# Performance work log

Measured on AMD Instinct MI355X. Metric: run time of the kernel, lower is better.

Reference implementation:

```python
import jax, jax.numpy as jnp
import numpy as np
from jax import lax

B, T, I, H, O = 256, 512, 64, 128, 2  # batch, seq_len, input_size, hidden_size, output_size


def gru_layer(x, Wih, Whh, bih, bhh, reverse):
    # x: [B,T,in_dim], Wih: [3H,in_dim], Whh: [3H,H]; PyTorch gate order: r, z, n
    xw = jnp.einsum('bti,gi->btg', x, Wih) + bih  # precompute input projections [B,T,3H]

    def step(h, xw_t):
        gh = h @ Whh.T + bhh  # [B,3H]
        r = jax.nn.sigmoid(xw_t[:, :H] + gh[:, :H])
        z = jax.nn.sigmoid(xw_t[:, H:2 * H] + gh[:, H:2 * H])
        n = jnp.tanh(xw_t[:, 2 * H:] + r * gh[:, 2 * H:])
        h_new = (1.0 - z) * n + z * h
        return h_new, h_new

    h0 = jnp.zeros((x.shape[0], H), x.dtype)
    _, hs = lax.scan(step, h0, jnp.swapaxes(xw, 0, 1), reverse=reverse)
    # lax.scan with reverse=True stacks outputs aligned to original time order,
    # matching PyTorch's bidirectional GRU output layout.
    return jnp.swapaxes(hs, 0, 1)  # [B,T,H]


def gru_forward(x, params, fc_w, fc_b):
    h = x
    for (Wf, Uf, bf, cf, Wb, Ub, bb, cb) in params:
        fwd = gru_layer(h, Wf, Uf, bf, cf, reverse=False)
        bwd = gru_layer(h, Wb, Ub, bb, cb, reverse=True)
        h = jnp.concatenate([fwd, bwd], axis=-1)  # [B,T,2H]
    last = jax.nn.relu(h[:, -1, :])  # relu then take last timestep (equivalent order)
    return last @ fc_w.T + fc_b  # [B,O]


def setup_inputs() -> dict:
    key = jax.random.key(0)
    ks = iter(jax.random.split(key, 24))
    s = 1.0 / np.sqrt(H)  # PyTorch GRU init scale
    u = lambda shape: jax.random.uniform(next(ks), shape, jnp.float32, -s, s)
    inp = {"x": jax.random.normal(next(ks), (B, T, I), jnp.float32)}
    for l, in_dim in enumerate([I, 2 * H]):
        for d in ("f", "b"):
            inp[f"Wih{l}{d}"] = u((3 * H, in_dim))
            inp[f"Whh{l}{d}"] = u((3 * H, H))
            inp[f"bih{l}{d}"] = u((3 * H,))
            inp[f"bhh{l}{d}"] = u((3 * H,))
    inp["fc_w"] = u((O, 2 * H))
    inp["fc_b"] = u((O,))
    return inp


def reference(x, Wih0f, Whh0f, bih0f, bhh0f, Wih0b, Whh0b, bih0b, bhh0b,
              Wih1f, Whh1f, bih1f, bhh1f, Wih1b, Whh1b, bih1b, bhh1b,
              fc_w, fc_b):
    params = [(Wih0f, Whh0f, bih0f, bhh0f, Wih0b, Whh0b, bih0b, bhh0b),
              (Wih1f, Whh1f, bih1f, bhh1f, Wih1b, Whh1b, bih1b, bhh1b)]
    return gru_forward(x, params, fc_w, fc_b)
```

## Files before the change

### kernel.cpp

```cpp
#include <hip/hip_runtime.h>
#include <hip/hip_fp16.h>

#define B_  256
#define T_  512
#define I_  64
#define H_  128
#define G_  384
#define HC  256

#define O_OUT0 0ull
#define O_XW1  67108864ull
#define O_X16  O_XW1
#define O_WP   167772160ull
#define O_H1F  (O_WP + 196608ull)
#define O_WF16 (O_H1F + 131072ull)

typedef _Float16 h8 __attribute__((ext_vector_type(8)));
typedef _Float16 h2 __attribute__((ext_vector_type(2)));
typedef float    f4 __attribute__((ext_vector_type(4)));

#define MFMA16 __builtin_amdgcn_mfma_f32_16x16x32_f16

__device__ __forceinline__ float sigm(float x)   { return __builtin_amdgcn_rcpf(1.f + __expf(-x)); }
__device__ __forceinline__ float tanh_f(float x) { return 1.f - 2.f * __builtin_amdgcn_rcpf(1.f + __expf(2.f * x)); }

__device__ __forceinline__ void bar_lds() {
    asm volatile("s_waitcnt lgkmcnt(0)\n\ts_barrier" ::: "memory");
}

__device__ __forceinline__ h8 load_w8(const float* src) {
    f4 a = *(const f4*)src;
    f4 b = *(const f4*)(src + 4);
    h8 v;
    v[0]=(_Float16)a[0]; v[1]=(_Float16)a[1]; v[2]=(_Float16)a[2]; v[3]=(_Float16)a[3];
    v[4]=(_Float16)b[0]; v[5]=(_Float16)b[1]; v[6]=(_Float16)b[2]; v[7]=(_Float16)b[3];
    return v;
}

__global__ void prep(const float* __restrict__ x, _Float16* __restrict__ x16,
                     const float* __restrict__ Wf, _Float16* __restrict__ wf16,
                     const float* __restrict__ W1b, __half2* __restrict__ wp) {
    const int bid = blockIdx.x;
    const int tid = threadIdx.x;
    if (bid < 4096) {
        int i = bid * 256 + tid;
        const float* s = x + (size_t)i * 8;
        f4 a = *(const f4*)s, b = *(const f4*)(s + 4);
        h8 v;
        v[0]=(_Float16)a[0]; v[1]=(_Float16)a[1]; v[2]=(_Float16)a[2]; v[3]=(_Float16)a[3];
        v[4]=(_Float16)b[0]; v[5]=(_Float16)b[1]; v[6]=(_Float16)b[2]; v[7]=(_Float16)b[3];
        *(h8*)(x16 + (size_t)i * 8) = v;
    } else if (bid < 4144) {
        int i = (bid - 4096) * 256 + tid;
        const float* s = Wf + (size_t)i * 8;
        f4 a = *(const f4*)s, b = *(const f4*)(s + 4);
        h8 v;
        v[0]=(_Float16)a[0]; v[1]=(_Float16)a[1]; v[2]=(_Float16)a[2]; v[3]=(_Float16)a[3];
        v[4]=(_Float16)b[0]; v[5]=(_Float16)b[1]; v[6]=(_Float16)b[2]; v[7]=(_Float16)b[3];
        *(h8*)(wf16 + (size_t)i * 8) = v;
    } else {
        int i = (bid - 4144) * 256 + tid;
        int c = i % G_;
        int k2 = i / G_;
        wp[i] = __halves2half2(__float2half(W1b[c * 256 + 2 * k2]),
                               __float2half(W1b[c * 256 + 2 * k2 + 1]));
    }
}

__launch_bounds__(512, 1)
__global__ void scan_l0(const _Float16* __restrict__ x16,
                        const float* __restrict__ Wih_f, const float* __restrict__ Whh_f,
                        const float* __restrict__ bih_f, const float* __restrict__ bhh_f,
                        const float* __restrict__ Wih_b, const float* __restrict__ Whh_b,
                        const float* __restrict__ bih_b, const float* __restrict__ bhh_b,
                        _Float16* __restrict__ out0) {
    __shared__ __align__(16) _Float16 s_h[2][16 * 128];

    const int tid  = threadIdx.x;
    const int lane = tid & 63;
    const int w    = tid >> 6;
    const int dir  = blockIdx.y;
    const int b0   = blockIdx.x * 4;

    const float* Wih = dir ? Wih_b : Wih_f;
    const float* Whh = dir ? Whh_b : Whh_f;
    const float* bih = dir ? bih_b : bih_f;
    const float* bhh = dir ? bhh_b : bhh_f;

    for (int i = tid; i < 2 * 16 * 128; i += 512) ((_Float16*)s_h)[i] = (_Float16)0.f;

    const int ln15 = lane & 15;
    const int lq   = lane >> 4;
    const int col  = 16 * w + ln15;

    h8 bh[3][4], bx[3][2];
    float seedR = bih[col] + bhh[col];
    float seedZ = bih[H_ + col] + bhh[H_ + col];
    float bihN  = bih[2 * H_ + col];
    float bhhN  = bhh[2 * H_ + col];
#pragma unroll
    for (int g = 0; g < 3; g++) {
        int n = g * H_ + col;
#pragma unroll
        for (int kt = 0; kt < 4; kt++) bh[g][kt] = load_w8(Whh + (size_t)n * H_ + kt * 32 + lq * 8);
#pragma unroll
        for (int kt = 0; kt < 2; kt++) bx[g][kt] = load_w8(Wih + (size_t)n * I_ + kt * 32 + lq * 8);
    }
    const int arow = ln15 & 12;
    int offh[4];
#pragma unroll
    for (int kt = 0; kt < 4; kt++)
        offh[kt] = arow * 128 + (((kt * 4 + lq) ^ arow) & 15) * 8;
    const int row0  = lq * 4;
    const int offw0 = row0 * 128 + ((((col >> 3) ^ row0) & 15)) * 8 + (col & 7);

    const _Float16* xbase = x16 + ((size_t)(b0 + (ln15 >> 2)) * T_) * I_ + lq * 8;

    const f4 z4 = (f4){0.f, 0.f, 0.f, 0.f};
    const f4 sR4 = (f4){seedR, seedR, seedR, seedR};
    const f4 sZ4 = (f4){seedZ, seedZ, seedZ, seedZ};
    const f4 sXn4 = (f4){bihN, bihN, bihN, bihN};
    const f4 sHn4 = (f4){bhhN, bhhN, bhhN, bhhN};

    _Float16* op = out0 + ((size_t)(b0 + lq) * T_ + (dir ? (T_ - 1) : 0)) * HC + dir * H_ + col;
    const int ostep = dir ? -HC : HC;
    const _Float16* xpA = xbase + (size_t)(dir ? (T_ - 4) : 3) * I_;
    const _Float16* xpB = xbase + (size_t)(dir ? (T_ - 5) : 4) * I_;
    const int xstep = dir ? -(2 * I_) : (2 * I_);

    float hF = 0.f;
    float xr0, xz0, xn0, xr1, xz1, xn1;
    h8 xvA0, xvA1, xvB0, xvB1;
    {
        int t0 = dir ? (T_ - 1) : 0;
        int t1 = dir ? (T_ - 2) : 1;
        int t2 = dir ? (T_ - 3) : 2;
        h8 xc0 = *(const h8*)(xbase + (size_t)t0 * I_);
        h8 xc1 = *(const h8*)(xbase + (size_t)t0 * I_ + 32);
        xvA0 = *(const h8*)(xbase + (size_t)t1 * I_);
        xvA1 = *(const h8*)(xbase + (size_t)t1 * I_ + 32);
        xvB0 = *(const h8*)(xbase + (size_t)t2 * I_);
        xvB1 = *(const h8*)(xbase + (size_t)t2 * I_ + 32);
        f4 aXr = sR4, aXz = sZ4, aXn = sXn4;
        aXr = MFMA16(xc0, bx[0][0], aXr, 0, 0, 0);
        aXz = MFMA16(xc0, bx[1][0], aXz, 0, 0, 0);
        aXn = MFMA16(xc0, bx[2][0], aXn, 0, 0, 0);
        aXr = MFMA16(xc1, bx[0][1], aXr, 0, 0, 0);
        aXz = MFMA16(xc1, bx[1][1], aXz, 0, 0, 0);
        aXn = MFMA16(xc1, bx[2][1], aXn, 0, 0, 0);
        xr0 = aXr[0]; xz0 = aXz[0]; xn0 = aXn[0];
    }
    __syncthreads();

#pragma unroll 1
    for (int t = 0; t < T_; t += 2) {
        {
            h8 ah0 = *(const h8*)&s_h[0][offh[0]];
            h8 ah1 = *(const h8*)&s_h[0][offh[1]];
            h8 ah2 = *(const h8*)&s_h[0][offh[2]];
            h8 ah3 = *(const h8*)&s_h[0][offh[3]];
            f4 hRa = z4, hRb = z4, hZa = z4, hZb = z4, hNa = sHn4, hNb = z4;
            hRa = MFMA16(ah0, bh[0][0], hRa, 0, 0, 0);
            hZa = MFMA16(ah0, bh[1][0], hZa, 0, 0, 0);
            hNa = MFMA16(ah0, bh[2][0], hNa, 0, 0, 0);
            hRb = MFMA16(ah2, bh[0][2], hRb, 0, 0, 0);
            hZb = MFMA16(ah2, bh[1][2], hZb, 0, 0, 0);
            hNb = MFMA16(ah2, bh[2][2], hNb, 0, 0, 0);
            hRa = MFMA16(ah1, bh[0][1], hRa, 0, 0, 0);
            hZa = MFMA16(ah1, bh[1][1], hZa, 0, 0, 0);
            hNa = MFMA16(ah1, bh[2][1], hNa, 0, 0, 0);
            hRb = MFMA16(ah3, bh[0][3], hRb, 0, 0, 0);
            hZb = MFMA16(ah3, bh[1][3], hZb, 0, 0, 0);
            hNb = MFMA16(ah3, bh[2][3], hNb, 0, 0, 0);
            float r = sigm(xr0 + hRa[0] + hRb[0]);
            float z = sigm(xz0 + hZa[0] + hZb[0]);
            float n = tanh_f(xn0 + r * (hNa[0] + hNb[0]));
            float h = n + z * (hF - n);
            hF = h;
            s_h[1][offw0] = (_Float16)h;
            *op = (_Float16)h; op += ostep;
            {
                f4 aXr = sR4, aXz = sZ4, aXn = sXn4;
                aXr = MFMA16(xvA0, bx[0][0], aXr, 0, 0, 0);
                aXz = MFMA16(xvA0, bx[1][0], aXz, 0, 0, 0);
                aXn = MFMA16(xvA0, bx[2][0], aXn, 0, 0, 0);
                aXr = MFMA16(xvA1, bx[0][1], aXr, 0, 0, 0);
                aXz = MFMA16(xvA1, bx[1][1], aXz, 0, 0, 0);
                aXn = MFMA16(xvA1, bx[2][1], aXn, 0, 0, 0);
                xr1 = aXr[0]; xz1 = aXz[0]; xn1 = aXn[0];
            }
            if (t + 3 < T_) {
                xvA0 = *(const h8*)(xpA);
                xvA1 = *(const h8*)(xpA + 32);
                xpA += xstep;
            }
            bar_lds();
        }
        {
            h8 ah0 = *(const h8*)&s_h[1][offh[0]];
            h8 ah1 = *(const h8*)&s_h[1][offh[1]];
            h8 ah2 = *(const h8*)&s_h[1][offh[2]];
            h8 ah3 = *(const h8*)&s_h[1][offh[3]];
            f4 hRa = z4, hRb = z4, hZa = z4, hZb = z4, hNa = sHn4, hNb = z4;
            hRa = MFMA16(ah0, bh[0][0], hRa, 0, 0, 0);
            hZa = MFMA16(ah0, bh[1][0], hZa, 0, 0, 0);
            hNa = MFMA16(ah0, bh[2][0], hNa, 0, 0, 0);
            hRb = MFMA16(ah2, bh[0][2], hRb, 0, 0, 0);
            hZb = MFMA16(ah2, bh[1][2], hZb, 0, 0, 0);
            hNb = MFMA16(ah2, bh[2][2], hNb, 0, 0, 0);
            hRa = MFMA16(ah1, bh[0][1], hRa, 0, 0, 0);
            hZa = MFMA16(ah1, bh[1][1], hZa, 0, 0, 0);
            hNa = MFMA16(ah1, bh[2][1], hNa, 0, 0, 0);
            hRb = MFMA16(ah3, bh[0][3], hRb, 0, 0, 0);
            hZb = MFMA16(ah3, bh[1][3], hZb, 0, 0, 0);
            hNb = MFMA16(ah3, bh[2][3], hNb, 0, 0, 0);
            float r = sigm(xr1 + hRa[0] + hRb[0]);
            float z = sigm(xz1 + hZa[0] + hZb[0]);
            float n = tanh_f(xn1 + r * (hNa[0] + hNb[0]));
            float h = n + z * (hF - n);
            hF = h;
            s_h[0][offw0] = (_Float16)h;
            *op = (_Float16)h; op += ostep;
            if (t + 2 < T_) {
                f4 aXr = sR4, aXz = sZ4, aXn = sXn4;
                aXr = MFMA16(xvB0, bx[0][0], aXr, 0, 0, 0);
                aXz = MFMA16(xvB0, bx[1][0], aXz, 0, 0, 0);
                aXn = MFMA16(xvB0, bx[2][0], aXn, 0, 0, 0);
                aXr = MFMA16(xvB1, bx[0][1], aXr, 0, 0, 0);
                aXz = MFMA16(xvB1, bx[1][1], aXz, 0, 0, 0);
                aXn = MFMA16(xvB1, bx[2][1], aXn, 0, 0, 0);
                xr0 = aXr[0]; xz0 = aXz[0]; xn0 = aXn[0];
            }
            if (t + 4 < T_) {
                xvB0 = *(const h8*)(xpB);
                xvB1 = *(const h8*)(xpB + 32);
                xpB += xstep;
            }
            bar_lds();
        }
    }
}

__launch_bounds__(256, 1)
__global__ void gemm_xw1(const _Float16* __restrict__ A,
                         const _Float16* __restrict__ Bw,
                         const float* __restrict__ bias,
                         _Float16* __restrict__ C) {
    __shared__ __align__(16) _Float16 sA[2][64 * 64];
    __shared__ __align__(16) _Float16 sB[2][384 * 64];
    const int tid  = threadIdx.x;
    const int lane = tid & 63;
    const int w    = tid >> 6;
    const int wm   = w & 1, wn = w >> 1;
    const int ln15 = lane & 15, lq = lane >> 4;
    const size_t m0 = (size_t)blockIdx.x * 64;

    f4 acc[2][12] = {};

    int aRow[2], aG[2], aOff[2];
#pragma unroll
    for (int k = 0; k < 2; k++) {
        int idx = k * 256 + tid;
        aRow[k] = idx >> 3; aG[k] = idx & 7;
        aOff[k] = aRow[k] * 64 + ((aG[k] ^ (aRow[k] & 7)) & 7) * 8;
    }
    int bRow[12], bG[12], bOff[12];
#pragma unroll
    for (int k = 0; k < 12; k++) {
        int idx = k * 256 + tid;
        bRow[k] = idx >> 3; bG[k] = idx & 7;
        bOff[k] = bRow[k] * 64 + ((bG[k] ^ (bRow[k] & 7)) & 7) * 8;
    }
    int offA[2][2], offB[12][2];
#pragma unroll
    for (int mt = 0; mt < 2; mt++)
#pragma unroll
        for (int kt = 0; kt < 2; kt++) {
            int row = wm * 32 + mt * 16 + ln15;
            offA[mt][kt] = row * 64 + (((kt * 4 + lq) ^ (row & 7)) & 7) * 8;
        }
#pragma unroll
    for (int nt = 0; nt < 12; nt++)
#pragma unroll
        for (int kt = 0; kt < 2; kt++) {
            int row = wn * 192 + nt * 16 + ln15;
            offB[nt][kt] = row * 64 + (((kt * 4 + lq) ^ (row & 7)) & 7) * 8;
        }

    {
        h8 av[2], bv[12];
#pragma unroll
        for (int k = 0; k < 2; k++) av[k] = *(const h8*)(A + (m0 + aRow[k]) * 256 + aG[k] * 8);
#pragma unroll
        for (int k = 0; k < 12; k++) bv[k] = *(const h8*)(Bw + (size_t)bRow[k] * 256 + bG[k] * 8);
#pragma unroll
        for (int k = 0; k < 2; k++) *(h8*)&sA[0][aOff[k]] = av[k];
#pragma unroll
        for (int k = 0; k < 12; k++) *(h8*)&sB[0][bOff[k]] = bv[k];
        bar_lds();
    }

#pragma unroll
    for (int c = 0; c < 4; c++) {
        const int cur = c & 1;
        h8 av[2], bv[12];
        if (c < 3) {
#pragma unroll
            for (int k = 0; k < 2; k++)
                av[k] = *(const h8*)(A + (m0 + aRow[k]) * 256 + (c + 1) * 64 + aG[k] * 8);
#pragma unroll
            for (int k = 0; k < 12; k++)
                bv[k] = *(const h8*)(Bw + (size_t)bRow[k] * 256 + (c + 1) * 64 + bG[k] * 8);
        }
#pragma unroll
        for (int kt = 0; kt < 2; kt++) {
            h8 af0 = *(const h8*)&sA[cur][offA[0][kt]];
            h8 af1 = *(const h8*)&sA[cur][offA[1][kt]];
#pragma unroll
            for (int nt = 0; nt < 12; nt++) {
                h8 bf = *(const h8*)&sB[cur][offB[nt][kt]];
                acc[0][nt] = MFMA16(af0, bf, acc[0][nt], 0, 0, 0);
                acc[1][nt] = MFMA16(af1, bf, acc[1][nt], 0, 0, 0);
            }
        }
        if (c < 3) {
#pragma unroll
            for (int k = 0; k < 2; k++) *(h8*)&sA[cur ^ 1][aOff[k]] = av[k];
#pragma unroll
            for (int k = 0; k < 12; k++) *(h8*)&sB[cur ^ 1][bOff[k]] = bv[k];
            bar_lds();
        }
    }
#pragma unroll
    for (int nt = 0; nt < 12; nt++) {
        int col = wn * 192 + nt * 16 + ln15;
        float bb = bias[col];
        int pcol = (col < 256) ? ((col & 127) * 2 + (col >> 7)) : col;
#pragma unroll
        for (int mt = 0; mt < 2; mt++) {
            size_t row = m0 + wm * 32 + mt * 16 + lq * 4;
#pragma unroll
            for (int reg = 0; reg < 4; reg++)
                C[(row + reg) * G_ + pcol] = (_Float16)(acc[mt][nt][reg] + bb);
        }
    }
}

__launch_bounds__(512, 1)
__global__ void scan_l1(const _Float16* __restrict__ xw1,
                        const float* __restrict__ Whh,
                        const float* __restrict__ bhh,
                        float* __restrict__ h1f) {
    __shared__ __align__(16) _Float16 s_h[2][16 * 128];

    const int tid  = threadIdx.x;
    const int lane = tid & 63;
    const int w    = tid >> 6;
    const int b0   = blockIdx.x * 4;

    for (int i = tid; i < 2 * 16 * 128; i += 512) ((_Float16*)s_h)[i] = (_Float16)0.f;

    const int ln15 = lane & 15;
    const int lq   = lane >> 4;
    const int col  = 16 * w + ln15;

    h8 bh[3][4];
    float bhhF[3];
#pragma unroll
    for (int g = 0; g < 3; g++) {
        int n = g * H_ + col;
        bhhF[g] = bhh[n];
#pragma unroll
        for (int kt = 0; kt < 4; kt++) bh[g][kt] = load_w8(Whh + (size_t)n * H_ + kt * 32 + lq * 8);
    }
    const int arow = ln15 & 12;
    int offh[4];
#pragma unroll
    for (int kt = 0; kt < 4; kt++)
        offh[kt] = arow * 128 + (((kt * 4 + lq) ^ arow) & 15) * 8;
    const int row0  = lq * 4;
    const int offw0 = row0 * 128 + ((((col >> 3) ^ row0) & 15)) * 8 + (col & 7);

    const _Float16* rzbase = xw1 + ((size_t)(b0 + lq) * T_) * G_ + 2 * col;
    const _Float16* nbase  = xw1 + ((size_t)(b0 + lq) * T_) * G_ + 256 + col;

    const f4 z4 = (f4){0.f, 0.f, 0.f, 0.f};
    const f4 sR4 = (f4){bhhF[0], bhhF[0], bhhF[0], bhhF[0]};
    const f4 sZ4 = (f4){bhhF[1], bhhF[1], bhhF[1], bhhF[1]};
    const f4 sN4 = (f4){bhhF[2], bhhF[2], bhhF[2], bhhF[2]};

    __syncthreads();

    float hF = 0.f;
    h2 rzA = *(const h2*)(rzbase);
    h2 rzB = *(const h2*)(rzbase + G_);
    _Float16 nA = *nbase;
    _Float16 nB = *(nbase + G_);
    const _Float16* rzP2 = rzbase + 2 * G_;
    const _Float16* nP2  = nbase  + 2 * G_;
    const _Float16* rzP3 = rzbase + 3 * G_;
    const _Float16* nP3  = nbase  + 3 * G_;

#pragma unroll 1
    for (int s = 0; s < T_; s += 2) {
        {
            h8 ah0 = *(const h8*)&s_h[0][offh[0]];
            h8 ah1 = *(const h8*)&s_h[0][offh[1]];
            h8 ah2 = *(const h8*)&s_h[0][offh[2]];
            h8 ah3 = *(const h8*)&s_h[0][offh[3]];
            float xr = (float)rzA[0], xz = (float)rzA[1], xn = (float)nA;
            if (s + 2 < T_) {
                rzA = *(const h2*)rzP2;
                nA  = *nP2;
                rzP2 += 2 * G_; nP2 += 2 * G_;
            }
            f4 hRa = sR4, hRb = z4, hZa = sZ4, hZb = z4, hNa = sN4, hNb = z4;
            hRa = MFMA16(ah0, bh[0][0], hRa, 0, 0, 0);
            hZa = MFMA16(ah0, bh[1][0], hZa, 0, 0, 0);
            hNa = MFMA16(ah0, bh[2][0], hNa, 0, 0, 0);
            hRb = MFMA16(ah2, bh[0][2], hRb, 0, 0, 0);
            hZb = MFMA16(ah2, bh[1][2], hZb, 0, 0, 0);
            hNb = MFMA16(ah2, bh[2][2], hNb, 0, 0, 0);
            hRa = MFMA16(ah1, bh[0][1], hRa, 0, 0, 0);
            hZa = MFMA16(ah1, bh[1][1], hZa, 0, 0, 0);
            hNa = MFMA16(ah1, bh[2][1], hNa, 0, 0, 0);
            hRb = MFMA16(ah3, bh[0][3], hRb, 0, 0, 0);
            hZb = MFMA16(ah3, bh[1][3], hZb, 0, 0, 0);
            hNb = MFMA16(ah3, bh[2][3], hNb, 0, 0, 0);
            float r = sigm(xr + hRa[0] + hRb[0]);
            float z = sigm(xz + hZa[0] + hZb[0]);
            float n = tanh_f(xn + r * (hNa[0] + hNb[0]));
            float h = n + z * (hF - n);
            hF = h;
            s_h[1][offw0] = (_Float16)h;
            bar_lds();
        }
        {
            h8 ah0 = *(const h8*)&s_h[1][offh[0]];
            h8 ah1 = *(const h8*)&s_h[1][offh[1]];
            h8 ah2 = *(const h8*)&s_h[1][offh[2]];
            h8 ah3 = *(const h8*)&s_h[1][offh[3]];
            float xr = (float)rzB[0], xz = (float)rzB[1], xn = (float)nB;
            if (s + 3 < T_) {
                rzB = *(const h2*)rzP3;
                nB  = *nP3;
                rzP3 += 2 * G_; nP3 += 2 * G_;
            }
            f4 hRa = sR4, hRb = z4, hZa = sZ4, hZb = z4, hNa = sN4, hNb = z4;
            hRa = MFMA16(ah0, bh[0][0], hRa, 0, 0, 0);
            hZa = MFMA16(ah0, bh[1][0], hZa, 0, 0, 0);
            hNa = MFMA16(ah0, bh[2][0], hNa, 0, 0, 0);
            hRb = MFMA16(ah2, bh[0][2], hRb, 0, 0, 0);
            hZb = MFMA16(ah2, bh[1][2], hZb, 0, 0, 0);
            hNb = MFMA16(ah2, bh[2][2], hNb, 0, 0, 0);
            hRa = MFMA16(ah1, bh[0][1], hRa, 0, 0, 0);
            hZa = MFMA16(ah1, bh[1][1], hZa, 0, 0, 0);
            hNa = MFMA16(ah1, bh[2][1], hNa, 0, 0, 0);
            hRb = MFMA16(ah3, bh[0][3], hRb, 0, 0, 0);
            hZb = MFMA16(ah3, bh[1][3], hZb, 0, 0, 0);
            hNb = MFMA16(ah3, bh[2][3], hNb, 0, 0, 0);
            float r = sigm(xr + hRa[0] + hRb[0]);
            float z = sigm(xz + hZa[0] + hZb[0]);
            float n = tanh_f(xn + r * (hNa[0] + hNb[0]));
            float h = n + z * (hF - n);
            hF = h;
            s_h[0][offw0] = (_Float16)h;
            bar_lds();
        }
    }
    h1f[(size_t)(b0 + lq) * H_ + col] = hF;
}

__launch_bounds__(384)
__global__ void final_k(const _Float16* __restrict__ out0,
                        const float* __restrict__ h1f,
                        const __half2* __restrict__ w1b,
                        const float* __restrict__ bih1b, const float* __restrict__ bhh1b,
                        const float* __restrict__ fcw, const float* __restrict__ fcb,
                        float* __restrict__ out) {
    __shared__ __align__(16) float s_x1[HC];
    __shared__ __align__(16) float s_xw[G_];
    __shared__ __align__(16) float s_hc[HC];
    __shared__ float s_red[8];
    const int tid = threadIdx.x;
    const int b = blockIdx.x;
    if (tid < HC)
        s_x1[tid] = (float)out0[((size_t)b * T_ + (T_ - 1)) * HC + tid];
    __syncthreads();
    {
        float acc0 = 0.f, acc1 = 0.f;
        const float2* xv = (const float2*)s_x1;
#pragma unroll 8
        for (int k2 = 0; k2 < 128; k2 += 2) {
            float2 w0 = __half22float2(w1b[k2 * G_ + tid]);
            float2 w1 = __half22float2(w1b[(k2 + 1) * G_ + tid]);
            float2 a0 = xv[k2], a1 = xv[k2 + 1];
            acc0 += a0.x * w0.x + a0.y * w0.y;
            acc1 += a1.x * w1.x + a1.y * w1.y;
        }
        s_xw[tid] = bih1b[tid] + acc0 + acc1;
    }
    __syncthreads();
    if (tid < H_) {
        int j = tid;
        float rg = sigm(s_xw[j] + bhh1b[j]);
        float zg = sigm(s_xw[H_ + j] + bhh1b[H_ + j]);
        float ng = tanh_f(s_xw[2 * H_ + j] + rg * bhh1b[2 * H_ + j]);
        float hb = (1.f - zg) * ng;
        s_hc[H_ + j] = fmaxf(hb, 0.f);
        s_hc[j] = fmaxf(h1f[(size_t)b * H_ + j], 0.f);
    }
    __syncthreads();
    if (tid < HC) {
        float hv = s_hc[tid];
        float p0 = hv * fcw[tid];
        float p1 = hv * fcw[HC + tid];
#pragma unroll
        for (int off = 32; off; off >>= 1) {
            p0 += __shfl_down(p0, off);
            p1 += __shfl_down(p1, off);
        }
        if ((tid & 63) == 0) { s_red[(tid >> 6) * 2] = p0; s_red[(tid >> 6) * 2 + 1] = p1; }
    }
    __syncthreads();
    if (tid == 0) {
        out[b * 2 + 0] = fcb[0] + s_red[0] + s_red[2] + s_red[4] + s_red[6];
        out[b * 2 + 1] = fcb[1] + s_red[1] + s_red[3] + s_red[5] + s_red[7];
    }
}

extern "C" void kernel_launch(void* const* d_in, const int* in_sizes, int n_in,
                              void* d_out, int out_size, void* d_ws, size_t ws_size,
                              hipStream_t stream) {
    (void)in_sizes; (void)n_in; (void)out_size; (void)ws_size;
    const float* x     = (const float*)d_in[0];
    const float* Wih0f = (const float*)d_in[1];
    const float* Whh0f = (const float*)d_in[2];
    const float* bih0f = (const float*)d_in[3];
    const float* bhh0f = (const float*)d_in[4];
    const float* Wih0b = (const float*)d_in[5];
    const float* Whh0b = (const float*)d_in[6];
    const float* bih0b = (const float*)d_in[7];
    const float* bhh0b = (const float*)d_in[8];
    const float* Wih1f = (const float*)d_in[9];
    const float* Whh1f = (const float*)d_in[10];
    const float* bih1f = (const float*)d_in[11];
    const float* bhh1f = (const float*)d_in[12];
    const float* Wih1b = (const float*)d_in[13];
    const float* bih1b = (const float*)d_in[15];
    const float* bhh1b = (const float*)d_in[16];
    const float* fcw   = (const float*)d_in[17];
    const float* fcb   = (const float*)d_in[18];

    char* ws = (char*)d_ws;
    _Float16* out0 = (_Float16*)(ws + O_OUT0);
    _Float16* xw1  = (_Float16*)(ws + O_XW1);
    _Float16* x16  = (_Float16*)(ws + O_X16);
    __half2*  wp   = (__half2*)(ws + O_WP);
    float*    h1f  = (float*)(ws + O_H1F);
    _Float16* wf16 = (_Float16*)(ws + O_WF16);
    float*    out  = (float*)d_out;

    prep<<<4336, 256, 0, stream>>>(x, x16, Wih1f, wf16, Wih1b, wp);

    scan_l0<<<dim3(64, 2), 512, 0, stream>>>(x16, Wih0f, Whh0f, bih0f, bhh0f,
                                             Wih0b, Whh0b, bih0b, bhh0b, out0);

    gemm_xw1<<<2048, 256, 0, stream>>>(out0, wf16, bih1f, xw1);

    scan_l1<<<64, 512, 0, stream>>>(xw1, Whh1f, bhh1f, h1f);

    final_k<<<256, 384, 0, stream>>>(out0, h1f, wp, bih1b, bhh1b, fcw, fcb, out);
}
```

Measured before the change: 576.0 us.

## Batch two timesteps per x-projection MFMA and halve scan_l1 waves

In scan_l0, the input-projection MFMA now packs rows from two consecutive timesteps into one 16x16 tile. Lanes pick their timestep by a bit of the lane index, and accumulator elements 0 and 2 are used, so one set of six MFMAs covers two steps instead of one. In scan_l1, each wave now computes two 16-column hidden tiles, so the block drops from 8 waves to 4. This cuts the wave count that takes part in every per-step barrier, at the cost of more per-wave MFMA work and register pressure on the serial recurrence path.

```diff
diff --git a/kernel.cpp b/kernel.cpp
--- a/kernel.cpp
+++ b/kernel.cpp
@@ -114,33 +114,28 @@
     const int row0  = lq * 4;
     const int offw0 = row0 * 128 + ((((col >> 3) ^ row0) & 15)) * 8 + (col & 7);
 
-    const _Float16* xbase = x16 + ((size_t)(b0 + (ln15 >> 2)) * T_) * I_ + lq * 8;
-
     const f4 z4 = (f4){0.f, 0.f, 0.f, 0.f};
     const f4 sR4 = (f4){seedR, seedR, seedR, seedR};
     const f4 sZ4 = (f4){seedZ, seedZ, seedZ, seedZ};
     const f4 sXn4 = (f4){bihN, bihN, bihN, bihN};
     const f4 sHn4 = (f4){bhhN, bhhN, bhhN, bhhN};
 
+    const int tbit = (ln15 >> 1) & 1;
+    const _Float16* xpb = x16 + ((size_t)(b0 + (ln15 >> 2)) * T_ + (dir ? (T_ - 1 - tbit) : tbit)) * I_ + lq * 8;
+    const int xIterStep = dir ? -(2 * I_) : (2 * I_);
+
     _Float16* op = out0 + ((size_t)(b0 + lq) * T_ + (dir ? (T_ - 1) : 0)) * HC + dir * H_ + col;
     const int ostep = dir ? -HC : HC;
-    const _Float16* xpA = xbase + (size_t)(dir ? (T_ - 4) : 3) * I_;
-    const _Float16* xpB = xbase + (size_t)(dir ? (T_ - 5) : 4) * I_;
-    const int xstep = dir ? -(2 * I_) : (2 * I_);
 
     float hF = 0.f;
-    float xr0, xz0, xn0, xr1, xz1, xn1;
-    h8 xvA0, xvA1, xvB0, xvB1;
+    float xrA, xzA, xnA, xrB, xzB, xnB;
+    float nxrA, nxzA, nxnA, nxrB, nxzB, nxnB;
+    h8 xv0, xv1;
     {
-        int t0 = dir ? (T_ - 1) : 0;
-        int t1 = dir ? (T_ - 2) : 1;
-        int t2 = dir ? (T_ - 3) : 2;
-        h8 xc0 = *(const h8*)(xbase + (size_t)t0 * I_);
-        h8 xc1 = *(const h8*)(xbase + (size_t)t0 * I_ + 32);
-        xvA0 = *(const h8*)(xbase + (size_t)t1 * I_);
-        xvA1 = *(const h8*)(xbase + (size_t)t1 * I_ + 32);
-        xvB0 = *(const h8*)(xbase + (size_t)t2 * I_);
-        xvB1 = *(const h8*)(xbase + (size_t)t2 * I_ + 32);
+        h8 xc0 = *(const h8*)(xpb);
+        h8 xc1 = *(const h8*)(xpb + 32);
+        xv0 = *(const h8*)(xpb + xIterStep);
+        xv1 = *(const h8*)(xpb + xIterStep + 32);
         f4 aXr = sR4, aXz = sZ4, aXn = sXn4;
         aXr = MFMA16(xc0, bx[0][0], aXr, 0, 0, 0);
         aXz = MFMA16(xc0, bx[1][0], aXz, 0, 0, 0);
@@ -148,8 +143,10 @@
         aXr = MFMA16(xc1, bx[0][1], aXr, 0, 0, 0);
         aXz = MFMA16(xc1, bx[1][1], aXz, 0, 0, 0);
         aXn = MFMA16(xc1, bx[2][1], aXn, 0, 0, 0);
-        xr0 = aXr[0]; xz0 = aXz[0]; xn0 = aXn[0];
-    }
+        xrA = aXr[0]; xzA = aXz[0]; xnA = aXn[0];
+        xrB = aXr[2]; xzB = aXz[2]; xnB = aXn[2];
+    }
+    const _Float16* xp = xpb + 2 * xIterStep;
     __syncthreads();
 
 #pragma unroll 1
@@ -172,27 +169,23 @@
             hRb = MFMA16(ah3, bh[0][3], hRb, 0, 0, 0);
             hZb = MFMA16(ah3, bh[1][3], hZb, 0, 0, 0);
             hNb = MFMA16(ah3, bh[2][3], hNb, 0, 0, 0);
-            float r = sigm(xr0 + hRa[0] + hRb[0]);
-            float z = sigm(xz0 + hZa[0] + hZb[0]);
-            float n = tanh_f(xn0 + r * (hNa[0] + hNb[0]));
+            float r = sigm(xrA + hRa[0] + hRb[0]);
+            float z = sigm(xzA + hZa[0] + hZb[0]);
+            float n = tanh_f(xnA + r * (hNa[0] + hNb[0]));
             float h = n + z * (hF - n);
             hF = h;
             s_h[1][offw0] = (_Float16)h;
             *op = (_Float16)h; op += ostep;
-            {
+            if (t + 2 < T_) {
                 f4 aXr = sR4, aXz = sZ4, aXn = sXn4;
-                aXr = MFMA16(xvA0, bx[0][0], aXr, 0, 0, 0);
-                aXz = MFMA16(xvA0, bx[1][0], aXz, 0, 0, 0);
-                aXn = MFMA16(xvA0, bx[2][0], aXn, 0, 0, 0);
-                aXr = MFMA16(xvA1, bx[0][1], aXr, 0, 0, 0);
-                aXz = MFMA16(xvA1, bx[1][1], aXz, 0, 0, 0);
-                aXn = MFMA16(xvA1, bx[2][1], aXn, 0, 0, 0);
-                xr1 = aXr[0]; xz1 = aXz[0]; xn1 = aXn[0];
-            }
-            if (t + 3 < T_) {
-                xvA0 = *(const h8*)(xpA);
-                xvA1 = *(const h8*)(xpA + 32);
-                xpA += xstep;
+                aXr = MFMA16(xv0, bx[0][0], aXr, 0, 0, 0);
+                aXz = MFMA16(xv0, bx[1][0], aXz, 0, 0, 0);
+                aXn = MFMA16(xv0, bx[2][0], aXn, 0, 0, 0);
+                aXr = MFMA16(xv1, bx[0][1], aXr, 0, 0, 0);
+                aXz = MFMA16(xv1, bx[1][1], aXz, 0, 0, 0);
+                aXn = MFMA16(xv1, bx[2][1], aXn, 0, 0, 0);
+                nxrA = aXr[0]; nxzA = aXz[0]; nxnA = aXn[0];
+                nxrB = aXr[2]; nxzB = aXz[2]; nxnB = aXn[2];
             }
             bar_lds();
         }
@@ -214,27 +207,19 @@
             hRb = MFMA16(ah3, bh[0][3], hRb, 0, 0, 0);
             hZb = MFMA16(ah3, bh[1][3], hZb, 0, 0, 0);
             hNb = MFMA16(ah3, bh[2][3], hNb, 0, 0, 0);
-            float r = sigm(xr1 + hRa[0] + hRb[0]);
-            float z = sigm(xz1 + hZa[0] + hZb[0]);
-            float n = tanh_f(xn1 + r * (hNa[0] + hNb[0]));
+            float r = sigm(xrB + hRa[0] + hRb[0]);
+            float z = sigm(xzB + hZa[0] + hZb[0]);
+            float n = tanh_f(xnB + r * (hNa[0] + hNb[0]));
             float h = n + z * (hF - n);
             hF = h;
             s_h[0][offw0] = (_Float16)h;
             *op = (_Float16)h; op += ostep;
-            if (t + 2 < T_) {
-                f4 aXr = sR4, aXz = sZ4, aXn = sXn4;
-                aXr = MFMA16(xvB0, bx[0][0], aXr, 0, 0, 0);
-                aXz = MFMA16(xvB0, bx[1][0], aXz, 0, 0, 0);
-                aXn = MFMA16(xvB0, bx[2][0], aXn, 0, 0, 0);
-                aXr = MFMA16(xvB1, bx[0][1], aXr, 0, 0, 0);
-                aXz = MFMA16(xvB1, bx[1][1], aXz, 0, 0, 0);
-                aXn = MFMA16(xvB1, bx[2][1], aXn, 0, 0, 0);
-                xr0 = aXr[0]; xz0 = aXz[0]; xn0 = aXn[0];
-            }
+            xrA = nxrA; xzA = nxzA; xnA = nxnA;
+            xrB = nxrB; xzB = nxzB; xnB = nxnB;
             if (t + 4 < T_) {
-                xvB0 = *(const h8*)(xpB);
-                xvB1 = *(const h8*)(xpB + 32);
-                xpB += xstep;
+                xv0 = *(const h8*)(xp);
+                xv1 = *(const h8*)(xp + 32);
+                xp += xIterStep;
             }
             bar_lds();
         }
@@ -346,7 +331,7 @@
     }
 }
 
-__launch_bounds__(512, 1)
+__launch_bounds__(256, 1)
 __global__ void scan_l1(const _Float16* __restrict__ xw1,
                         const float* __restrict__ Whh,
                         const float* __restrict__ bhh,
@@ -358,48 +343,74 @@
     const int w    = tid >> 6;
     const int b0   = blockIdx.x * 4;
 
-    for (int i = tid; i < 2 * 16 * 128; i += 512) ((_Float16*)s_h)[i] = (_Float16)0.f;
+    for (int i = tid; i < 2 * 16 * 128; i += 256) ((_Float16*)s_h)[i] = (_Float16)0.f;
 
     const int ln15 = lane & 15;
     const int lq   = lane >> 4;
-    const int col  = 16 * w + ln15;
-
-    h8 bh[3][4];
-    float bhhF[3];
-#pragma unroll
-    for (int g = 0; g < 3; g++) {
-        int n = g * H_ + col;
-        bhhF[g] = bhh[n];
-#pragma unroll
-        for (int kt = 0; kt < 4; kt++) bh[g][kt] = load_w8(Whh + (size_t)n * H_ + kt * 32 + lq * 8);
-    }
+    int col[2];
+    col[0] = 32 * w + ln15;
+    col[1] = 32 * w + 16 + ln15;
+
+    h8 bh[3][4][2];
+    float bhhF[3][2];
+#pragma unroll
+    for (int g = 0; g < 3; g++)
+#pragma unroll
+        for (int ct = 0; ct < 2; ct++) {
+            int n = g * H_ + col[ct];
+            bhhF[g][ct] = bhh[n];
+#pragma unroll
+            for (int kt = 0; kt < 4; kt++)
+                bh[g][kt][ct] = load_w8(Whh + (size_t)n * H_ + kt * 32 + lq * 8);
+        }
     const int arow = ln15 & 12;
     int offh[4];
 #pragma unroll
     for (int kt = 0; kt < 4; kt++)
         offh[kt] = arow * 128 + (((kt * 4 + lq) ^ arow) & 15) * 8;
-    const int row0  = lq * 4;
-    const int offw0 = row0 * 128 + ((((col >> 3) ^ row0) & 15)) * 8 + (col & 7);
-
-    const _Float16* rzbase = xw1 + ((size_t)(b0 + lq) * T_) * G_ + 2 * col;
-    const _Float16* nbase  = xw1 + ((size_t)(b0 + lq) * T_) * G_ + 256 + col;
+    const int row0 = lq * 4;
+    int offw[2];
+#pragma unroll
+    for (int ct = 0; ct < 2; ct++)
+        offw[ct] = row0 * 128 + ((((col[ct] >> 3) ^ row0) & 15)) * 8 + (col[ct] & 7);
 
     const f4 z4 = (f4){0.f, 0.f, 0.f, 0.f};
-    const f4 sR4 = (f4){bhhF[0], bhhF[0], bhhF[0], bhhF[0]};
-    const f4 sZ4 = (f4){bhhF[1], bhhF[1], bhhF[1], bhhF[1]};
-    const f4 sN4 = (f4){bhhF[2], bhhF[2], bhhF[2], bhhF[2]};
+    f4 sR[2], sZ[2], sN[2];
+#pragma unroll
+    for (int ct = 0; ct < 2; ct++) {
+        sR[ct] = (f4){bhhF[0][ct], bhhF[0][ct], bhhF[0][ct], bhhF[0][ct]};
+        sZ[ct] = (f4){bhhF[1][ct], bhhF[1][ct], bhhF[1][ct], bhhF[1][ct]};
+        sN[ct] = (f4){bhhF[2][ct], bhhF[2][ct], bhhF[2][ct], bhhF[2][ct]};
+    }
+
+    const _Float16* rzbase[2];
+    const _Float16* nbase[2];
+#pragma unroll
+    for (int ct = 0; ct < 2; ct++) {
+        rzbase[ct] = xw1 + ((size_t)(b0 + lq) * T_) * G_ + 2 * col[ct];
+        nbase[ct]  = xw1 + ((size_t)(b0 + lq) * T_) * G_ + 256 + col[ct];
+    }
 
     __syncthreads();
 
-    float hF = 0.f;
-    h2 rzA = *(const h2*)(rzbase);
-    h2 rzB = *(const h2*)(rzbase + G_);
-    _Float16 nA = *nbase;
-    _Float16 nB = *(nbase + G_);
-    const _Float16* rzP2 = rzbase + 2 * G_;
-    const _Float16* nP2  = nbase  + 2 * G_;
-    const _Float16* rzP3 = rzbase + 3 * G_;
-    const _Float16* nP3  = nbase  + 3 * G_;
+    float hF[2] = {0.f, 0.f};
+    h2 rzA[2], rzB[2];
+    _Float16 nA[2], nB[2];
+    const _Float16* rzP2[2];
+    const _Float16* nP2[2];
+    const _Float16* rzP3[2];
+    const _Float16* nP3[2];
+#pragma unroll
+    for (int ct = 0; ct < 2; ct++) {
+        rzA[ct] = *(const h2*)(rzbase[ct]);
+        rzB[ct] = *(const h2*)(rzbase[ct] + G_);
+        nA[ct]  = *nbase[ct];
+        nB[ct]  = *(nbase[ct] + G_);
+        rzP2[ct] = rzbase[ct] + 2 * G_;
+        nP2[ct]  = nbase[ct]  + 2 * G_;
+        rzP3[ct] = rzbase[ct] + 3 * G_;
+        nP3[ct]  = nbase[ct]  + 3 * G_;
+    }
 
 #pragma unroll 1
     for (int s = 0; s < T_; s += 2) {
@@ -408,31 +419,39 @@
             h8 ah1 = *(const h8*)&s_h[0][offh[1]];
             h8 ah2 = *(const h8*)&s_h[0][offh[2]];
             h8 ah3 = *(const h8*)&s_h[0][offh[3]];
-            float xr = (float)rzA[0], xz = (float)rzA[1], xn = (float)nA;
-            if (s + 2 < T_) {
-                rzA = *(const h2*)rzP2;
-                nA  = *nP2;
-                rzP2 += 2 * G_; nP2 += 2 * G_;
+            f4 hRa[2], hRb[2], hZa[2], hZb[2], hNa[2], hNb[2];
+            float xr[2], xz[2], xn[2];
+#pragma unroll
+            for (int ct = 0; ct < 2; ct++) {
+                xr[ct] = (float)rzA[ct][0]; xz[ct] = (float)rzA[ct][1]; xn[ct] = (float)nA[ct];
+                if (s + 2 < T_) {
+                    rzA[ct] = *(const h2*)rzP2[ct];
+                    nA[ct]  = *nP2[ct];
+                    rzP2[ct] += 2 * G_; nP2[ct] += 2 * G_;
+                }
+                hRa[ct] = sR[ct]; hRb[ct] = z4; hZa[ct] = sZ[ct]; hZb[ct] = z4; hNa[ct] = sN[ct]; hNb[ct] = z4;
+                hRa[ct] = MFMA16(ah0, bh[0][0][ct], hRa[ct], 0, 0, 0);
+                hZa[ct] = MFMA16(ah0, bh[1][0][ct], hZa[ct], 0, 0, 0);
+                hNa[ct] = MFMA16(ah0, bh[2][0][ct], hNa[ct], 0, 0, 0);
+                hRb[ct] = MFMA16(ah2, bh[0][2][ct], hRb[ct], 0, 0, 0);
+                hZb[ct] = MFMA16(ah2, bh[1][2][ct], hZb[ct], 0, 0, 0);
+                hNb[ct] = MFMA16(ah2, bh[2][2][ct], hNb[ct], 0, 0, 0);
+                hRa[ct] = MFMA16(ah1, bh[0][1][ct], hRa[ct], 0, 0, 0);
+                hZa[ct] = MFMA16(ah1, bh[1][1][ct], hZa[ct], 0, 0, 0);
+                hNa[ct] = MFMA16(ah1, bh[2][1][ct], hNa[ct], 0, 0, 0);
+                hRb[ct] = MFMA16(ah3, bh[0][3][ct], hRb[ct], 0, 0, 0);
+                hZb[ct] = MFMA16(ah3, bh[1][3][ct], hZb[ct], 0, 0, 0);
+                hNb[ct] = MFMA16(ah3, bh[2][3][ct], hNb[ct], 0, 0, 0);
             }
-            f4 hRa = sR4, hRb = z4, hZa = sZ4, hZb = z4, hNa = sN4, hNb = z4;
-            hRa = MFMA16(ah0, bh[0][0], hRa, 0, 0, 0);
-            hZa = MFMA16(ah0, bh[1][0], hZa, 0, 0, 0);
-            hNa = MFMA16(ah0, bh[2][0], hNa, 0, 0, 0);
-            hRb = MFMA16(ah2, bh[0][2], hRb, 0, 0, 0);
-            hZb = MFMA16(ah2, bh[1][2], hZb, 0, 0, 0);
-            hNb = MFMA16(ah2, bh[2][2], hNb, 0, 0, 0);
-            hRa = MFMA16(ah1, bh[0][1], hRa, 0, 0, 0);
-            hZa = MFMA16(ah1, bh[1][1], hZa, 0, 0, 0);
-            hNa = MFMA16(ah1, bh[2][1], hNa, 0, 0, 0);
-            hRb = MFMA16(ah3, bh[0][3], hRb, 0, 0, 0);
-            hZb = MFMA16(ah3, bh[1][3], hZb, 0, 0, 0);
-            hNb = MFMA16(ah3, bh[2][3], hNb, 0, 0, 0);
-            float r = sigm(xr + hRa[0] + hRb[0]);
-            float z = sigm(xz + hZa[0] + hZb[0]);
-            float n = tanh_f(xn + r * (hNa[0] + hNb[0]));
-            float h = n + z * (hF - n);
-            hF = h;
-            s_h[1][offw0] = (_Float16)h;
+#pragma unroll
+            for (int ct = 0; ct < 2; ct++) {
+                float r = sigm(xr[ct] + hRa[ct][0] + hRb[ct][0]);
+                float z = sigm(xz[ct] + hZa[ct][0] + hZb[ct][0]);
+                float n = tanh_f(xn[ct] + r * (hNa[ct][0] + hNb[ct][0]));
+                float h = n + z * (hF[ct] - n);
+                hF[ct] = h;
+                s_h[1][offw[ct]] = (_Float16)h;
+            }
             bar_lds();
         }
         {
@@ -440,35 +459,45 @@
             h8 ah1 = *(const h8*)&s_h[1][offh[1]];
             h8 ah2 = *(const h8*)&s_h[1][offh[2]];
             h8 ah3 = *(const h8*)&s_h[1][offh[3]];
-            float xr = (float)rzB[0], xz = (float)rzB[1], xn = (float)nB;
-            if (s + 3 < T_) {
-                rzB = *(const h2*)rzP3;
-                nB  = *nP3;
-                rzP3 += 2 * G_; nP3 += 2 * G_;
+            f4 hRa[2], hRb[2], hZa[2], hZb[2], hNa[2], hNb[2];
+            float xr[2], xz[2], xn[2];
+#pragma unroll
+            for (int ct = 0; ct < 2; ct++) {
+                xr[ct] = (float)rzB[ct][0]; xz[ct] = (float)rzB[ct][1]; xn[ct] = (float)nB[ct];
+                if (s + 3 < T_) {
+                    rzB[ct] = *(const h2*)rzP3[ct];
+                    nB[ct]  = *nP3[ct];
+                    rzP3[ct] += 2 * G_; nP3[ct] += 2 * G_;
+                }
+                hRa[ct] = sR[ct]; hRb[ct] = z4; hZa[ct] = sZ[ct]; hZb[ct] = z4; hNa[ct] = sN[ct]; hNb[ct] = z4;
+                hRa[ct] = MFMA16(ah0, bh[0][0][ct], hRa[ct], 0, 0, 0);
+                hZa[ct] = MFMA16(ah0, bh[1][0][ct], hZa[ct], 0, 0, 0);
+                hNa[ct] = MFMA16(ah0, bh[2][0][ct], hNa[ct], 0, 0, 0);
+                hRb[ct] = MFMA16(ah2, bh[0][2][ct], hRb[ct], 0, 0, 0);
+                hZb[ct] = MFMA16(ah2, bh[1][2][ct], hZb[ct], 0, 0, 0);
+                hNb[ct] = MFMA16(ah2, bh[2][2][ct], hNb[ct], 0, 0, 0);
+                hRa[ct] = MFMA16(ah1, bh[0][1][ct], hRa[ct], 0, 0, 0);
+                hZa[ct] = MFMA16(ah1, bh[1][1][ct], hZa[ct], 0, 0, 0);
+                hNa[ct] = MFMA16(ah1, bh[2][1][ct], hNa[ct], 0, 0, 0);
+                hRb[ct] = MFMA16(ah3, bh[0][3][ct], hRb[ct], 0, 0, 0);
+                hZb[ct] = MFMA16(ah3, bh[1][3][ct], hZb[ct], 0, 0, 0);
+                hNb[ct] = MFMA16(ah3, bh[2][3][ct], hNb[ct], 0, 0, 0);
             }
-            f4 hRa = sR4, hRb = z4, hZa = sZ4, hZb = z4, hNa = sN4, hNb = z4;
-            hRa = MFMA16(ah0, bh[0][0], hRa, 0, 0, 0);
-            hZa = MFMA16(ah0, bh[1][0], hZa, 0, 0, 0);
-            hNa = MFMA16(ah0, bh[2][0], hNa, 0, 0, 0);
-            hRb = MFMA16(ah2, bh[0][2], hRb, 0, 0, 0);
-            hZb = MFMA16(ah2, bh[1][2], hZb, 0, 0, 0);
-            hNb = MFMA16(ah2, bh[2][2], hNb, 0, 0, 0);
-            hRa = MFMA16(ah1, bh[0][1], hRa, 0, 0, 0);
-            hZa = MFMA16(ah1, bh[1][1], hZa, 0, 0, 0);
-            hNa = MFMA16(ah1, bh[2][1], hNa, 0, 0, 0);
-            hRb = MFMA16(ah3, bh[0][3], hRb, 0, 0, 0);
-            hZb = MFMA16(ah3, bh[1][3], hZb, 0, 0, 0);
-            hNb = MFMA16(ah3, bh[2][3], hNb, 0, 0, 0);
-            float r = sigm(xr + hRa[0] + hRb[0]);
-            float z = sigm(xz + hZa[0] + hZb[0]);
-            float n = tanh_f(xn + r * (hNa[0] + hNb[0]));
-            float h = n + z * (hF - n);
-            hF = h;
-            s_h[0][offw0] = (_Float16)h;
+#pragma unroll
+            for (int ct = 0; ct < 2; ct++) {
+                float r = sigm(xr[ct] + hRa[ct][0] + hRb[ct][0]);
+                float z = sigm(xz[ct] + hZa[ct][0] + hZb[ct][0]);
+                float n = tanh_f(xn[ct] + r * (hNa[ct][0] + hNb[ct][0]));
+                float h = n + z * (hF[ct] - n);
+                hF[ct] = h;
+                s_h[0][offw[ct]] = (_Float16)h;
+            }
             bar_lds();
         }
     }
-    h1f[(size_t)(b0 + lq) * H_ + col] = hF;
+#pragma unroll
+    for (int ct = 0; ct < 2; ct++)
+        h1f[(size_t)(b0 + lq) * H_ + col[ct]] = hF[ct];
 }
 
 __launch_bounds__(384)
@@ -568,7 +597,7 @@
 
     gemm_xw1<<<2048, 256, 0, stream>>>(out0, wf16, bih1f, xw1);
 
-    scan_l1<<<64, 512, 0, stream>>>(xw1, Whh1f, bhh1f, h1f);
+    scan_l1<<<64, 256, 0, stream>>>(xw1, Whh1f, bhh1f, h1f);
 
     final_k<<<256, 384, 0, stream>>>(out0, h1f, wp, bih1b, bhh1b, fcw, fcb, out);
 }
```

Result: slower. 641.7 us (+11.4%).
